# Kernel optimization log

Hardware: AMD Instinct MI355X
Metric: run time of the kernel (lower is better)

Reference implementation:

```python
import jax, jax.numpy as jnp
import numpy as np

B, S, D, H, HD = 4, 2048, 1024, 16, 64


def setup_inputs() -> dict:
    key = jax.random.key(0)
    ks = jax.random.split(key, 5)
    x = jax.random.normal(ks[0], (B, S, D), dtype=jnp.float32)
    padding_mask = jnp.ones((B, S), dtype=bool)
    # GPT-2-style init scales
    W_attn = jax.random.normal(ks[1], (D, 3, H, HD), dtype=jnp.float32) * (1.0 / np.sqrt(D))
    b_attn = jnp.zeros((3, H, HD), dtype=jnp.float32)
    W_proj = jax.random.normal(ks[2], (H, HD, D), dtype=jnp.float32) * (1.0 / np.sqrt(D))
    b_proj = jnp.zeros((D,), dtype=jnp.float32)
    return {"x": x, "padding_mask": padding_mask, "W_attn": W_attn,
            "b_attn": b_attn, "W_proj": W_proj, "b_proj": b_proj}


def reference(x, padding_mask, W_attn, b_attn, W_proj, b_proj):
    # fused QKV projection: [B,S,D] x [D,3,H,HD] -> [B,3,H,S,HD]
    qkv = jnp.einsum('bsd,dqhk->bqhsk', x, W_attn) + b_attn[None, :, :, None, :].transpose(0, 1, 2, 3, 4)
    q, k, v = qkv[:, 0], qkv[:, 1], qkv[:, 2]  # each [B,H,S,HD]
    scale = 1.0 / jnp.sqrt(jnp.asarray(HD, dtype=x.dtype))
    # scores over (query position s, key position t)
    scores = jnp.einsum('bhsk,bhtk->bhst', q, k) * scale
    causal = jnp.tril(jnp.ones((S, S), dtype=bool))  # [S_query, S_key]
    mask = causal[None, None, :, :] & padding_mask[:, None, None, :]
    masked = jnp.where(mask, scores, -jnp.inf)
    attn = jax.nn.softmax(masked, axis=-1)  # dropout rate is 0.0
    out = jnp.einsum('bhst,bhtk->bhsk', attn, v)
    return jnp.einsum('bhsk,hkd->bsd', out, W_proj) + b_proj
```

## Files before the change

kernel.cpp:

```cpp
#include <hip/hip_runtime.h>
#include <hip/hip_bf16.h>
#include <math.h>


typedef short bf16x8 __attribute__((ext_vector_type(8)));
typedef float f32x4 __attribute__((ext_vector_type(4)));
typedef float f32x16 __attribute__((ext_vector_type(16)));
typedef unsigned short ushort8v __attribute__((ext_vector_type(8)));

#define MFMA16(a,b,c) __builtin_amdgcn_mfma_f32_16x16x32_bf16(a,b,c,0,0,0)
#define MFMA32(a,b,c) __builtin_amdgcn_mfma_f32_32x32x16_bf16(a,b,c,0,0,0)

__device__ __forceinline__ void gload16(const void* g, void* l) {
    __builtin_amdgcn_global_load_lds((const __attribute__((address_space(1))) void*)g,
                                     (__attribute__((address_space(3))) void*)l, 16, 0, 0);
}

__device__ __forceinline__ unsigned short f2bf(float f) {
    unsigned int u = __float_as_uint(f);
    u += 0x7fffu + ((u >> 16) & 1u);
    return (unsigned short)(u >> 16);
}

__device__ __forceinline__ int cvtpk(float a, float b) {
    int r;
    asm("v_cvt_pk_bf16_f32 %0, %1, %2" : "=v"(r) : "v"(a), "v"(b));
    return r;
}

__device__ __forceinline__ float exp2a(float x) {
    float r;
    asm("v_exp_f32 %0, %1" : "=v"(r) : "v"(x));
    return r;
}

__device__ __forceinline__ float max3f(float a, float b, float c) {
    float r;
    asm("v_max3_f32 %0, %1, %2, %3" : "=v"(r) : "v"(a), "v"(b), "v"(c));
    return r;
}

#define QSCALE 0.18033688011112042f

__global__ __launch_bounds__(256) void convert_x(const float* __restrict__ src,
                                                 unsigned short* __restrict__ dst) {
    int idx = (blockIdx.x * 256 + threadIdx.x) * 4;
    float4 v = *(const float4*)&src[idx];
    ushort4 o;
    o.x = f2bf(v.x); o.y = f2bf(v.y); o.z = f2bf(v.z); o.w = f2bf(v.w);
    *(ushort4*)&dst[idx] = o;
}

__global__ __launch_bounds__(256) void convert_wt(const float* __restrict__ src,
                                                  unsigned short* __restrict__ dst, int N) {
    __shared__ float T[64][65];
    const int t = threadIdx.x;
    const int n0 = blockIdx.x * 64, k0 = blockIdx.y * 64;
    #pragma unroll
    for (int i = 0; i < 4; i++) {
        int row = (t >> 4) + 16 * i;
        int c4 = t & 15;
        float4 v = *(const float4*)&src[(size_t)(k0 + row) * N + n0 + c4 * 4];
        T[row][c4 * 4 + 0] = v.x; T[row][c4 * 4 + 1] = v.y;
        T[row][c4 * 4 + 2] = v.z; T[row][c4 * 4 + 3] = v.w;
    }
    __syncthreads();
    #pragma unroll
    for (int i = 0; i < 4; i++) {
        int n = (t >> 4) + 16 * i;
        int k4 = (t & 15) * 4;
        ushort4 o;
        o.x = f2bf(T[k4 + 0][n]); o.y = f2bf(T[k4 + 1][n]);
        o.z = f2bf(T[k4 + 2][n]); o.w = f2bf(T[k4 + 3][n]);
        *(ushort4*)&dst[(size_t)(n0 + n) * 1024 + k0 + k4] = o;
    }
}

template<int MODE>
__global__ __launch_bounds__(256) void gemm_mfma(
        const unsigned short* __restrict__ A, const unsigned short* __restrict__ Bt,
        const float* __restrict__ bias,
        unsigned short* __restrict__ Qp, unsigned short* __restrict__ Kp,
        unsigned short* __restrict__ Vp, float* __restrict__ OUT) {
    __shared__ __align__(16) unsigned short Al[2][128 * 32];
    __shared__ __align__(16) unsigned short Bl[2][128 * 32];
    const int tid = threadIdx.x;
    const int l = tid & 63, w = tid >> 6;
    const int wm = w >> 1, wn = w & 1;
    const int m0 = blockIdx.y * 128, n0 = blockIdx.x * 128;
    const int l15 = l & 15, l4 = l >> 4;

    f32x4 acc[4][4] = {};

    int bb = 0, s0 = 0;
    if (MODE == 1) { bb = m0 >> 11; s0 = m0 & 2047; }

    auto stage = [&](int buf, int k0) {
        #pragma unroll
        for (int p = 0; p < 2; p++) {
            int idx = tid + 256 * p;
            int row = idx >> 2, sl = idx & 3;
            int gc = sl ^ (row & 3);
            const unsigned short* ga;
            if (MODE == 0) {
                ga = A + (size_t)(m0 + row) * 1024 + k0 + gc * 8;
            } else {
                int h = k0 >> 6;
                ga = A + ((size_t)(bb * 16 + h) * 2048 + s0 + row) * 64 + (k0 & 63) + gc * 8;
            }
            gload16(ga, (char*)Al[buf] + w * 1024 + p * 4096);
            const unsigned short* gb = Bt + (size_t)(n0 + row) * 1024 + k0 + gc * 8;
            gload16(gb, (char*)Bl[buf] + w * 1024 + p * 4096);
        }
    };

    stage(0, 0);
    __syncthreads();

    for (int t = 0; t < 32; t++) {
        const int buf = t & 1;
        if (t < 31) stage(buf ^ 1, (t + 1) * 32);

        bf16x8 af[4], bfr[4];
        #pragma unroll
        for (int mi = 0; mi < 4; mi++) {
            int row = 64 * wm + 16 * mi + l15;
            af[mi] = *(const bf16x8*)((const char*)Al[buf] + row * 64 + ((l4 ^ (l15 & 3)) * 16));
        }
        #pragma unroll
        for (int ni = 0; ni < 4; ni++) {
            int row = 64 * wn + 16 * ni + l15;
            bfr[ni] = *(const bf16x8*)((const char*)Bl[buf] + row * 64 + ((l4 ^ (l15 & 3)) * 16));
        }
        __builtin_amdgcn_s_setprio(1);
        #pragma unroll
        for (int mi = 0; mi < 4; mi++)
            #pragma unroll
            for (int ni = 0; ni < 4; ni++)
                acc[mi][ni] = MFMA16(af[mi], bfr[ni], acc[mi][ni]);
        __builtin_amdgcn_s_setprio(0);

        __syncthreads();
    }

    if (MODE == 0) {
        const int qsel = n0 >> 10;
        unsigned short* dst = (qsel == 0) ? Qp : (qsel == 1) ? Kp : Vp;
        const float scale = (qsel == 0) ? QSCALE : 1.0f;
        const int h = ((n0 + 64 * wn) >> 6) & 15;
        #pragma unroll
        for (int ni = 0; ni < 4; ni++) {
            const int hd = 16 * ni + l15;
            const int ng = n0 + 64 * wn + hd;
            const float bv = bias[ng];
            #pragma unroll
            for (int mi = 0; mi < 4; mi++) {
                #pragma unroll
                for (int bi = 0; bi < 4; bi++) {
                    int m = m0 + 64 * wm + 16 * mi + 4 * l4 + bi;
                    int b_ = m >> 11, s = m & 2047;
                    float v = (acc[mi][ni][bi] + bv) * scale;
                    dst[((size_t)(b_ * 16 + h) * 2048 + s) * 64 + hd] = f2bf(v);
                }
            }
        }
    } else {
        #pragma unroll
        for (int ni = 0; ni < 4; ni++) {
            const int ng = n0 + 64 * wn + 16 * ni + l15;
            const float bv = bias[ng];
            #pragma unroll
            for (int mi = 0; mi < 4; mi++) {
                #pragma unroll
                for (int bi = 0; bi < 4; bi++) {
                    int m = m0 + 64 * wm + 16 * mi + 4 * l4 + bi;
                    OUT[(size_t)m * 1024 + ng] = acc[mi][ni][bi] + bv;
                }
            }
        }
    }
}

__global__ __launch_bounds__(512, 4) void attn_mfma(
        const unsigned short* __restrict__ Q, const unsigned short* __restrict__ K,
        const unsigned short* __restrict__ V, unsigned short* __restrict__ AO) {
    __shared__ __align__(16) char smem[18432];
    unsigned short* Vl = (unsigned short*)(smem + 8192);
    const int tid = threadIdx.x;
    const int l = tid & 63, w = tid >> 6;
    const int hi = l >> 5, q31 = l & 31;
    const int bh = blockIdx.x & 63;
    const int g = blockIdx.x >> 6;
    const int pid = (g < 4) ? g : 11 - g;
    const int qi = (w >= 4) ? (15 - pid) : pid;
    const int q0 = qi * 128 + 32 * (w & 3);
    const int qg = q0 + q31;
    const unsigned short* qb = Q + (size_t)bh * 2048 * 64;
    const unsigned short* kb = K + (size_t)bh * 2048 * 64;
    const unsigned short* vb = V + (size_t)bh * 2048 * 64;
    unsigned short* ob = AO + (size_t)bh * 2048 * 64;

    bf16x8 qf[4];
    #pragma unroll
    for (int kk = 0; kk < 4; kk++)
        qf[kk] = *(const bf16x8*)&qb[(size_t)qg * 64 + 16 * kk + 8 * hi];

    f32x16 oa[2] = {};
    float mx = -INFINITY, ls = 0.0f;

    const int TMAX = 32 - 2 * pid;
    #pragma unroll 1
    for (int t = 0; t < TMAX; t++) {
        const int kv0 = 64 * t;
        __syncthreads();
        if (w >= 4) {
            int t2 = tid - 256;
            #pragma unroll
            for (int p = 0; p < 2; p++) {
                int idx = t2 + 256 * p;
                int row = idx >> 3, sl = idx & 7;
                gload16(kb + (size_t)(kv0 + row) * 64 + ((sl ^ (row & 7)) * 8),
                        smem + (w - 4) * 1024 + p * 4096);
            }
        } else {
            int kg = tid >> 3, hg = tid & 7;
            ushort8v v0 = *(const ushort8v*)&vb[(size_t)(kv0 + 2 * kg) * 64 + hg * 8];
            ushort8v v1 = *(const ushort8v*)&vb[(size_t)(kv0 + 2 * kg + 1) * 64 + hg * 8];
            #pragma unroll
            for (int i = 0; i < 8; i++) {
                int j = (i + tid) & 7;
                unsigned int pk = (unsigned int)(unsigned short)v0[j] |
                                  ((unsigned int)(unsigned short)v1[j] << 16);
                *(unsigned int*)((char*)Vl + (hg * 8 + j) * 144 + kg * 4) = pk;
            }
        }
        __syncthreads();

        #pragma unroll
        for (int st = 0; st < 2; st++) {
            const int k0g = kv0 + 32 * st;
            if (k0g <= q0 + 31) {
                f32x16 sa = {};
                __builtin_amdgcn_s_setprio(1);
                #pragma unroll
                for (int kk = 0; kk < 4; kk++) {
                    bf16x8 kf = *(const bf16x8*)((const char*)smem +
                        (32 * st + q31) * 128 + (((2 * kk + hi) ^ (l & 7)) * 16));
                    sa = MFMA32(kf, qf[kk], sa);
                }
                __builtin_amdgcn_s_setprio(0);
                float sv[16];
                #pragma unroll
                for (int r = 0; r < 16; r++) sv[r] = sa[r];
                if (k0g + 31 > q0) {
                    #pragma unroll
                    for (int r = 0; r < 16; r++) {
                        int key = k0g + (r & 3) + 8 * (r >> 2) + 4 * hi;
                        if (key > qg) sv[r] = -INFINITY;
                    }
                }
                float m16 = max3f(sv[0], sv[1], sv[2]);
                m16 = max3f(m16, sv[3], sv[4]);
                m16 = max3f(m16, sv[5], sv[6]);
                m16 = max3f(m16, sv[7], sv[8]);
                m16 = max3f(m16, sv[9], sv[10]);
                m16 = max3f(m16, sv[11], sv[12]);
                m16 = max3f(m16, sv[13], sv[14]);
                m16 = fmaxf(m16, sv[15]);
                float mo = fmaxf(m16, __shfl_xor(m16, 32));
                if (!__all(mo <= mx + 8.0f)) {
                    float mn = fmaxf(mx, mo);
                    float sc = exp2a(mx - mn);
                    mx = mn;
                    ls *= sc;
                    oa[0] *= sc;
                    oa[1] *= sc;
                }
                float ps = 0.0f;
                #pragma unroll
                for (int r = 0; r < 16; r++) { sv[r] = exp2a(sv[r] - mx); ps += sv[r]; }
                ls += ps + __shfl_xor(ps, 32);
                int pw[2][4];
                #pragma unroll
                for (int mm = 0; mm < 2; mm++) {
                    int x0 = cvtpk(sv[8 * mm + 0], sv[8 * mm + 1]);
                    int x1 = cvtpk(sv[8 * mm + 2], sv[8 * mm + 3]);
                    int y0 = cvtpk(sv[8 * mm + 4], sv[8 * mm + 5]);
                    int y1 = cvtpk(sv[8 * mm + 6], sv[8 * mm + 7]);
                    int sx0 = __shfl_xor(x0, 32), sx1 = __shfl_xor(x1, 32);
                    int sy0 = __shfl_xor(y0, 32), sy1 = __shfl_xor(y1, 32);
                    pw[mm][0] = hi ? sy0 : x0;
                    pw[mm][1] = hi ? sy1 : x1;
                    pw[mm][2] = hi ? y0 : sx0;
                    pw[mm][3] = hi ? y1 : sx1;
                }
                __builtin_amdgcn_s_setprio(1);
                #pragma unroll
                for (int ch = 0; ch < 2; ch++) {
                    #pragma unroll
                    for (int mm = 0; mm < 2; mm++) {
                        int hd = 32 * ch + q31;
                        bf16x8 vf = *(const bf16x8*)((const char*)Vl +
                            hd * 144 + (32 * st + 16 * mm + 8 * hi) * 2);
                        union { int i[4]; bf16x8 v; } pu;
                        pu.i[0] = pw[mm][0]; pu.i[1] = pw[mm][1];
                        pu.i[2] = pw[mm][2]; pu.i[3] = pw[mm][3];
                        oa[ch] = MFMA32(vf, pu.v, oa[ch]);
                    }
                }
                __builtin_amdgcn_s_setprio(0);
            }
        }
    }

    float inv = 1.0f / ls;
    oa[0] *= inv;
    oa[1] *= inv;
    __syncthreads();
    #pragma unroll 1
    for (int pass = 0; pass < 2; pass++) {
        if ((w >> 2) == pass) {
            unsigned short* Ol = (unsigned short*)(smem + (w & 3) * 4608);
            #pragma unroll
            for (int ch = 0; ch < 2; ch++)
                #pragma unroll
                for (int r = 0; r < 16; r++) {
                    int hd = (r & 3) + 8 * (r >> 2) + 4 * hi + 32 * ch;
                    Ol[q31 * 72 + hd] = f2bf(oa[ch][r]);
                }
            asm volatile("s_waitcnt lgkmcnt(0)" ::: "memory");
            int row = l >> 1;
            #pragma unroll
            for (int c = 0; c < 4; c++) {
                int col = (4 * (l & 1) + c) * 8;
                bf16x8 ov = *(const bf16x8*)((const char*)Ol + row * 144 + col * 2);
                *(bf16x8*)&ob[(size_t)(q0 + row) * 64 + col] = ov;
            }
        }
        __syncthreads();
    }
}

extern "C" void kernel_launch(void* const* d_in, const int* in_sizes, int n_in,
                              void* d_out, int out_size, void* d_ws, size_t ws_size,
                              hipStream_t stream) {
    const float* x      = (const float*)d_in[0];
    const float* W_attn = (const float*)d_in[2];
    const float* b_attn = (const float*)d_in[3];
    const float* W_proj = (const float*)d_in[4];
    const float* b_proj = (const float*)d_in[5];
    float* out = (float*)d_out;

    char* ws = (char*)d_ws;
    unsigned short* Xb  = (unsigned short*)(ws);
    unsigned short* Wat = (unsigned short*)(ws + 16777216);
    unsigned short* Wpt = (unsigned short*)(ws + 23068672);
    unsigned short* Qb  = (unsigned short*)(ws + 25165824);
    unsigned short* Kb  = (unsigned short*)(ws + 41943040);
    unsigned short* Vb  = (unsigned short*)(ws + 58720256);
    unsigned short* AOb = (unsigned short*)(ws + 75497472);

    convert_x<<<8192, 256, 0, stream>>>(x, Xb);
    convert_wt<<<dim3(48, 16), 256, 0, stream>>>(W_attn, Wat, 3072);
    convert_wt<<<dim3(16, 16), 256, 0, stream>>>(W_proj, Wpt, 1024);

    gemm_mfma<0><<<dim3(24, 64), 256, 0, stream>>>(Xb, Wat, b_attn, Qb, Kb, Vb, nullptr);
    attn_mfma<<<512, 512, 0, stream>>>(Qb, Kb, Vb, AOb);
    gemm_mfma<1><<<dim3(8, 64), 256, 0, stream>>>(AOb, Wpt, b_proj, nullptr, nullptr, nullptr, out);
}
```

Baseline: 273.5 us.

## Double-buffer K/V tiles in attention and deepen GEMM prefetch with explicit waitcnt

The GEMM loop now prefetches two stages ahead and swaps __syncthreads for explicit vmcnt waits plus raw barriers, so global loads overlap the MFMA work. The attention kernel double-buffers K and V in LDS, roughly doubling shared memory. It prefetches the next K tile asynchronously and holds the next V tile in registers, writing it transposed into the other LDS buffer after the compute barrier. This hides load latency behind compute, at the cost of more LDS per block, which may lower occupancy, and fragile hand-written waitcnt counts.

```diff
diff --git a/kernel.cpp b/kernel.cpp
--- a/kernel.cpp
+++ b/kernel.cpp
@@ -115,11 +115,15 @@
     };
 
     stage(0, 0);
-    __syncthreads();
-
+    stage(1, 32);
+
+    #pragma unroll 1
     for (int t = 0; t < 32; t++) {
         const int buf = t & 1;
-        if (t < 31) stage(buf ^ 1, (t + 1) * 32);
+        if (t < 31) asm volatile("s_waitcnt vmcnt(4)" ::: "memory");
+        else        asm volatile("s_waitcnt vmcnt(0)" ::: "memory");
+        __builtin_amdgcn_s_barrier();
+        asm volatile("" ::: "memory");
 
         bf16x8 af[4], bfr[4];
         #pragma unroll
@@ -140,7 +144,9 @@
                 acc[mi][ni] = MFMA16(af[mi], bfr[ni], acc[mi][ni]);
         __builtin_amdgcn_s_setprio(0);
 
-        __syncthreads();
+        asm volatile("" ::: "memory");
+        __builtin_amdgcn_s_barrier();
+        if (t < 30) stage(buf, (t + 2) * 32);
     }
 
     if (MODE == 0) {
@@ -184,8 +190,7 @@
 __global__ __launch_bounds__(512, 4) void attn_mfma(
         const unsigned short* __restrict__ Q, const unsigned short* __restrict__ K,
         const unsigned short* __restrict__ V, unsigned short* __restrict__ AO) {
-    __shared__ __align__(16) char smem[18432];
-    unsigned short* Vl = (unsigned short*)(smem + 8192);
+    __shared__ __align__(16) char smem[34816];
     const int tid = threadIdx.x;
     const int l = tid & 63, w = tid >> 6;
     const int hi = l >> 5, q31 = l & 31;
@@ -209,42 +214,70 @@
     float mx = -INFINITY, ls = 0.0f;
 
     const int TMAX = 32 - 2 * pid;
+
+    const int kg = tid >> 3, hg = tid & 7;
+    const int t2 = tid & 255;
+
+    auto stageK = [&](int t, char* dst) {
+        #pragma unroll
+        for (int p = 0; p < 2; p++) {
+            int idx = t2 + 256 * p;
+            int row = idx >> 3, sl = idx & 7;
+            gload16(kb + (size_t)(64 * t + row) * 64 + ((sl ^ (row & 7)) * 8),
+                    dst + (w - 4) * 1024 + p * 4096);
+        }
+    };
+    ushort8v va, vbr;
+    auto loadV = [&](int t) {
+        va  = *(const ushort8v*)&vb[(size_t)(64 * t + 2 * kg) * 64 + hg * 8];
+        vbr = *(const ushort8v*)&vb[(size_t)(64 * t + 2 * kg + 1) * 64 + hg * 8];
+    };
+    auto writeV = [&](char* Vdst) {
+        #pragma unroll
+        for (int i = 0; i < 8; i++) {
+            int j = (i + tid) & 7;
+            unsigned int pk = (unsigned int)(unsigned short)va[j] |
+                              ((unsigned int)(unsigned short)vbr[j] << 16);
+            *(unsigned int*)(Vdst + (hg * 8 + j) * 144 + kg * 4) = pk;
+        }
+    };
+
+    if (w >= 4) {
+        stageK(0, smem);
+    } else {
+        loadV(0);
+        asm volatile("s_waitcnt vmcnt(0)" ::: "memory");
+        writeV(smem + 16384);
+        asm volatile("s_waitcnt lgkmcnt(0)" ::: "memory");
+    }
+
     #pragma unroll 1
     for (int t = 0; t < TMAX; t++) {
-        const int kv0 = 64 * t;
-        __syncthreads();
+        const int cur = t & 1;
+        char* Kcur = smem + cur * 8192;
+        char* Vcur = smem + 16384 + cur * 9216;
         if (w >= 4) {
-            int t2 = tid - 256;
-            #pragma unroll
-            for (int p = 0; p < 2; p++) {
-                int idx = t2 + 256 * p;
-                int row = idx >> 3, sl = idx & 7;
-                gload16(kb + (size_t)(kv0 + row) * 64 + ((sl ^ (row & 7)) * 8),
-                        smem + (w - 4) * 1024 + p * 4096);
+            if (t + 1 < TMAX) {
+                stageK(t + 1, smem + (cur ^ 1) * 8192);
+                asm volatile("s_waitcnt vmcnt(2)" ::: "memory");
+            } else {
+                asm volatile("s_waitcnt vmcnt(0)" ::: "memory");
             }
         } else {
-            int kg = tid >> 3, hg = tid & 7;
-            ushort8v v0 = *(const ushort8v*)&vb[(size_t)(kv0 + 2 * kg) * 64 + hg * 8];
-            ushort8v v1 = *(const ushort8v*)&vb[(size_t)(kv0 + 2 * kg + 1) * 64 + hg * 8];
-            #pragma unroll
-            for (int i = 0; i < 8; i++) {
-                int j = (i + tid) & 7;
-                unsigned int pk = (unsigned int)(unsigned short)v0[j] |
-                                  ((unsigned int)(unsigned short)v1[j] << 16);
-                *(unsigned int*)((char*)Vl + (hg * 8 + j) * 144 + kg * 4) = pk;
-            }
-        }
-        __syncthreads();
+            if (t + 1 < TMAX) loadV(t + 1);
+        }
+        __builtin_amdgcn_s_barrier();
+        asm volatile("" ::: "memory");
 
         #pragma unroll
         for (int st = 0; st < 2; st++) {
-            const int k0g = kv0 + 32 * st;
+            const int k0g = 64 * t + 32 * st;
             if (k0g <= q0 + 31) {
                 f32x16 sa = {};
                 __builtin_amdgcn_s_setprio(1);
                 #pragma unroll
                 for (int kk = 0; kk < 4; kk++) {
-                    bf16x8 kf = *(const bf16x8*)((const char*)smem +
+                    bf16x8 kf = *(const bf16x8*)(Kcur +
                         (32 * st + q31) * 128 + (((2 * kk + hi) ^ (l & 7)) * 16));
                     sa = MFMA32(kf, qf[kk], sa);
                 }
@@ -300,7 +333,7 @@
                     #pragma unroll
                     for (int mm = 0; mm < 2; mm++) {
                         int hd = 32 * ch + q31;
-                        bf16x8 vf = *(const bf16x8*)((const char*)Vl +
+                        bf16x8 vf = *(const bf16x8*)(Vcur +
                             hd * 144 + (32 * st + 16 * mm + 8 * hi) * 2);
                         union { int i[4]; bf16x8 v; } pu;
                         pu.i[0] = pw[mm][0]; pu.i[1] = pw[mm][1];
@@ -310,6 +343,14 @@
                 }
                 __builtin_amdgcn_s_setprio(0);
             }
+        }
+
+        asm volatile("" ::: "memory");
+        __builtin_amdgcn_s_barrier();
+        if (w < 4 && t + 1 < TMAX) {
+            asm volatile("s_waitcnt vmcnt(0)" ::: "memory");
+            writeV(smem + 16384 + (cur ^ 1) * 9216);
+            asm volatile("s_waitcnt lgkmcnt(0)" ::: "memory");
         }
     }
 
```

Result: faster. 263.0 us (-3.9%).
